# Performance work log

Hardware: AMD Instinct MI355X
Metric: run time of the kernel (lower is better)

The kernel has to match this reference:

```python
import jax, jax.numpy as jnp
import numpy as np

NUM_HEADS = 16
HEAD_SIZE = 64
EMB = NUM_HEADS * HEAD_SIZE
B, S = 2, 2048


def setup_inputs() -> dict:
    key = jax.random.key(0)
    ks = jax.random.split(key, 8)
    return {
        "values": jax.random.normal(ks[0], (B, S, EMB), dtype=jnp.float32),
        "keys": jax.random.normal(ks[1], (B, S, EMB), dtype=jnp.float32),
        "queries": jax.random.normal(ks[2], (B, S, EMB), dtype=jnp.float32),
        "mask": jnp.ones((B, 1, 1, S), dtype=jnp.int32),
        "Wq": jax.random.normal(ks[3], (HEAD_SIZE, HEAD_SIZE), dtype=jnp.float32) / np.sqrt(HEAD_SIZE),
        "Wk": jax.random.normal(ks[4], (HEAD_SIZE, HEAD_SIZE), dtype=jnp.float32) / np.sqrt(HEAD_SIZE),
        "Wv": jax.random.normal(ks[5], (HEAD_SIZE, HEAD_SIZE), dtype=jnp.float32) / np.sqrt(HEAD_SIZE),
        "Wout": jax.random.normal(ks[6], (EMB, EMB), dtype=jnp.float32) / np.sqrt(EMB),
        "bout": jax.random.normal(ks[7], (EMB,), dtype=jnp.float32) * 0.01,
    }


def reference(values, keys, queries, mask, Wq, Wk, Wv, Wout, bout):
    n, q_len, E = queries.shape
    H, D = NUM_HEADS, HEAD_SIZE
    # split heads: [n, len, H, D]
    v = values.reshape(n, -1, H, D)
    k = keys.reshape(n, -1, H, D)
    q = queries.reshape(n, q_len, H, D)
    # per-head shared linears (torch Linear: x @ W.T), no bias
    v = jnp.einsum("nkhd,cd->nkhc", v, Wv)
    k = jnp.einsum("nkhd,cd->nkhc", k, Wk)
    q = jnp.einsum("nqhd,cd->nqhc", q, Wq)
    # scores: [n, H, q, k]
    energy = jnp.einsum("nqhd,nkhd->nhqk", q, k)
    energy = jnp.where(mask == 0, jnp.float32(-1e28), energy)
    # NOTE: source scales by sqrt(embedding_size), not head_size
    attn = jax.nn.softmax(energy / jnp.sqrt(jnp.float32(E)), axis=3)
    out = jnp.einsum("nhqk,nkhd->nqhd", attn, v).reshape(n, q_len, E)
    return out @ Wout.T + bout
```

## Files before the change

kernel.cpp:

```cpp
#include <hip/hip_runtime.h>
#include <hip/hip_bf16.h>


#define NHB 16
#define HS  64
#define EMB 1024
#define BB  2
#define SS  2048
#define NT  (SS / 64)

typedef __bf16 bf16_t;
typedef bf16_t bf16x8 __attribute__((ext_vector_type(8)));
typedef bf16_t bf16x4 __attribute__((ext_vector_type(4)));
typedef float  f32x4  __attribute__((ext_vector_type(4)));

__device__ __forceinline__ f32x4 mfma16(bf16x8 a, bf16x8 b, f32x4 c) {
    return __builtin_amdgcn_mfma_f32_16x16x32_bf16(a, b, c, 0, 0, 0);
}

__global__ __launch_bounds__(256) void proj_kernel(
    const float* __restrict__ queries, const float* __restrict__ keys,
    const float* __restrict__ values,
    const float* __restrict__ Wq, const float* __restrict__ Wk,
    const float* __restrict__ Wv,
    bf16_t* __restrict__ Qb, bf16_t* __restrict__ Kb, bf16_t* __restrict__ Vt)
{
    __shared__ bf16_t Ws[3][64][72];
    __shared__ bf16_t Xs[64][72];

    const int tid  = threadIdx.x;
    const int wave = tid >> 6, lane = tid & 63;
    const int q4 = lane >> 4, l16 = lane & 15;
    const int s0 = blockIdx.x * 64;
    const int h  = blockIdx.y, n = blockIdx.z;

    for (int mW = 0; mW < 3; ++mW) {
        const float* wp = (mW == 0) ? Wq : (mW == 1) ? Wk : Wv;
        #pragma unroll
        for (int i = 0; i < 4; ++i) {
            int idx4 = i * 256 + tid;
            float4 v = ((const float4*)wp)[idx4];
            int r = idx4 >> 4, c = (idx4 & 15) * 4;
            Ws[mW][r][c+0] = (bf16_t)v.x; Ws[mW][r][c+1] = (bf16_t)v.y;
            Ws[mW][r][c+2] = (bf16_t)v.z; Ws[mW][r][c+3] = (bf16_t)v.w;
        }
    }

    const size_t headBase = (size_t)(n * NHB + h) * SS * HS;

    for (int p = 0; p < 3; ++p) {
        __syncthreads();
        const float* xp = (p == 0) ? queries : (p == 1) ? keys : values;
        #pragma unroll
        for (int i = 0; i < 4; ++i) {
            int idx4 = i * 256 + tid;
            int r = idx4 >> 4, c = (idx4 & 15) * 4;
            float4 v = *(const float4*)&xp[((size_t)(n * SS + s0 + r)) * EMB + h * HS + c];
            Xs[r][c+0] = (bf16_t)v.x; Xs[r][c+1] = (bf16_t)v.y;
            Xs[r][c+2] = (bf16_t)v.z; Xs[r][c+3] = (bf16_t)v.w;
        }
        __syncthreads();

        bf16x8 xf[2], wf[4][2];
        #pragma unroll
        for (int kk = 0; kk < 2; ++kk)
            xf[kk] = *(const bf16x8*)&Xs[wave * 16 + l16][kk * 32 + q4 * 8];
        #pragma unroll
        for (int ct = 0; ct < 4; ++ct)
            #pragma unroll
            for (int kk = 0; kk < 2; ++kk)
                wf[ct][kk] = *(const bf16x8*)&Ws[p][ct * 16 + l16][kk * 32 + q4 * 8];

        if (p < 2) {
            bf16_t* dst = (p == 0) ? Qb : Kb;
            const float sc = (p == 0) ? (0.03125f * 1.44269504f) : 1.0f;
            #pragma unroll
            for (int ct = 0; ct < 4; ++ct) {
                f32x4 acc = {};
                acc = mfma16(wf[ct][0], xf[0], acc);
                acc = mfma16(wf[ct][1], xf[1], acc);
                bf16x4 pk;
                #pragma unroll
                for (int i = 0; i < 4; ++i) pk[i] = (bf16_t)(acc[i] * sc);
                *(bf16x4*)&dst[headBase + (size_t)(s0 + wave * 16 + l16) * HS
                               + ct * 16 + q4 * 4] = pk;
            }
        } else {
            #pragma unroll
            for (int ct = 0; ct < 4; ++ct) {
                f32x4 acc = {};
                acc = mfma16(xf[0], wf[ct][0], acc);
                acc = mfma16(xf[1], wf[ct][1], acc);
                bf16x4 pk;
                #pragma unroll
                for (int i = 0; i < 4; ++i) pk[i] = (bf16_t)acc[i];
                *(bf16x4*)&Vt[headBase + (size_t)(ct * 16 + l16) * SS
                              + s0 + (wave >> 1) * 32 + q4 * 8 + (wave & 1) * 4] = pk;
            }
        }
    }
}

__global__ __launch_bounds__(256) void attn_kernel(
    const bf16_t* __restrict__ Qb, const bf16_t* __restrict__ Kb,
    const bf16_t* __restrict__ Vt, const int* __restrict__ mask,
    bf16_t* __restrict__ Og)
{
    __shared__ bf16_t Ks[2][64][72];
    __shared__ bf16_t Vs[2][64][72];
    __shared__ float  Ms[2][64];

    const int tid = threadIdx.x;
    const int w = tid >> 6, lane = tid & 63;
    const int q4 = lane >> 4, l16 = lane & 15;
    const int qt = blockIdx.x, h = blockIdx.y, n = blockIdx.z;
    const size_t headBase = (size_t)(n * NHB + h) * SS * HS;
    const int* mrow = mask + n * SS;

    const int sr0 = tid >> 3, sc0 = (tid & 7) * 8;
    const int sr1 = sr0 + 32;
    const bf16_t* kb0 = Kb + headBase + (size_t)sr0 * HS + sc0;
    const bf16_t* kb1 = Kb + headBase + (size_t)sr1 * HS + sc0;
    const bf16_t* vt0 = Vt + headBase + (size_t)sr0 * SS + sc0;
    const bf16_t* vt1 = Vt + headBase + (size_t)sr1 * SS + sc0;

    bf16x8 bq[2][2];
    #pragma unroll
    for (int st = 0; st < 2; ++st) {
        const bf16_t* qptr = Qb + headBase
            + (size_t)(qt * 128 + w * 32 + st * 16 + l16) * HS;
        bq[st][0] = *(const bf16x8*)&qptr[q4 * 8];
        bq[st][1] = *(const bf16x8*)&qptr[32 + q4 * 8];
    }

    f32x4 oaccT[2][4] = {};
    float lsum[2] = {0.f, 0.f};

    *(bf16x8*)&Ks[0][sr0][sc0] = *(const bf16x8*)kb0;
    *(bf16x8*)&Ks[0][sr1][sc0] = *(const bf16x8*)kb1;
    *(bf16x8*)&Vs[0][sr0][sc0] = *(const bf16x8*)vt0;
    *(bf16x8*)&Vs[0][sr1][sc0] = *(const bf16x8*)vt1;
    if (tid < 64) Ms[0][tid] = mrow[tid] ? 1.0f : 0.0f;
    __syncthreads();

    for (int kt = 0; kt < NT; ++kt) {
        const int cur = kt & 1;
        const bool has_next = (kt + 1) < NT;
        bf16x8 gk0, gk1, gv0, gv1; float gm = 0.f;
        if (has_next) {
            const int k0n = (kt + 1) * 64;
            gk0 = *(const bf16x8*)(kb0 + (size_t)k0n * HS);
            gk1 = *(const bf16x8*)(kb1 + (size_t)k0n * HS);
            gv0 = *(const bf16x8*)(vt0 + k0n);
            gv1 = *(const bf16x8*)(vt1 + k0n);
            if (tid < 64) gm = mrow[k0n + tid] ? 1.0f : 0.0f;
        }

        f32x4 sacc[2][4] = {};
        #pragma unroll
        for (int ct = 0; ct < 4; ++ct) {
            bf16x8 ak0 = *(const bf16x8*)&Ks[cur][ct * 16 + l16][q4 * 8];
            bf16x8 ak1 = *(const bf16x8*)&Ks[cur][ct * 16 + l16][32 + q4 * 8];
            #pragma unroll
            for (int st = 0; st < 2; ++st) {
                sacc[st][ct] = mfma16(ak0, bq[st][0], sacc[st][ct]);
                sacc[st][ct] = mfma16(ak1, bq[st][1], sacc[st][ct]);
            }
        }

        bf16x4 pv[2][4];
        #pragma unroll
        for (int ct = 0; ct < 4; ++ct) {
            float mf[4];
            *(float4*)mf = *(const float4*)&Ms[cur][ct * 16 + q4 * 4];
            #pragma unroll
            for (int st = 0; st < 2; ++st) {
                bf16x4 pk;
                #pragma unroll
                for (int j = 0; j < 4; ++j) {
                    float e = exp2f(sacc[st][ct][j]) * mf[j];
                    lsum[st] += e;
                    pk[j] = (bf16_t)e;
                }
                pv[st][ct] = pk;
            }
        }

        #pragma unroll
        for (int kb = 0; kb < 2; ++kb) {
            bf16x8 pa[2];
            #pragma unroll
            for (int st = 0; st < 2; ++st)
                pa[st] = __builtin_shufflevector(pv[st][2 * kb], pv[st][2 * kb + 1],
                                                 0, 1, 2, 3, 4, 5, 6, 7);
            #pragma unroll
            for (int dt = 0; dt < 4; ++dt) {
                bf16x8 av = *(const bf16x8*)&Vs[cur][dt * 16 + l16][kb * 32 + q4 * 8];
                #pragma unroll
                for (int st = 0; st < 2; ++st)
                    oaccT[st][dt] = mfma16(av, pa[st], oaccT[st][dt]);
            }
        }

        if (has_next) {
            const int nxt = 1 - cur;
            *(bf16x8*)&Ks[nxt][sr0][sc0] = gk0;
            *(bf16x8*)&Ks[nxt][sr1][sc0] = gk1;
            *(bf16x8*)&Vs[nxt][sr0][sc0] = gv0;
            *(bf16x8*)&Vs[nxt][sr1][sc0] = gv1;
            if (tid < 64) Ms[nxt][tid] = gm;
        }
        __syncthreads();
    }

    #pragma unroll
    for (int st = 0; st < 2; ++st) {
        float ls = lsum[st];
        ls += __shfl_xor(ls, 16, 64);
        ls += __shfl_xor(ls, 32, 64);
        const float inv = 1.f / ls;
        const int qrow = qt * 128 + w * 32 + st * 16 + l16;
        bf16_t* obase = Og + ((size_t)(n * SS + qrow)) * EMB + h * HS;
        #pragma unroll
        for (int dt = 0; dt < 4; ++dt) {
            bf16x4 ov;
            #pragma unroll
            for (int j = 0; j < 4; ++j) ov[j] = (bf16_t)(oaccT[st][dt][j] * inv);
            *(bf16x4*)&obase[dt * 16 + q4 * 4] = ov;
        }
    }
}

__global__ __launch_bounds__(256) void wconv_kernel(
    const float* __restrict__ W, bf16_t* __restrict__ Wb)
{
    int idx4 = blockIdx.x * 256 + threadIdx.x;
    float4 v = ((const float4*)W)[idx4];
    bf16x4 o;
    o[0] = (bf16_t)v.x; o[1] = (bf16_t)v.y; o[2] = (bf16_t)v.z; o[3] = (bf16_t)v.w;
    *(bf16x4*)&Wb[idx4 * 4] = o;
}

__global__ __launch_bounds__(512) void outproj_kernel(
    const bf16_t* __restrict__ Og, const bf16_t* __restrict__ Wb,
    const float* __restrict__ bout, float* __restrict__ out)
{
    __shared__ bf16_t As[2][128][72];
    __shared__ bf16_t Bs[2][128][72];
    const int tid = threadIdx.x;
    const int w = tid >> 6, lane = tid & 63;
    const int q4 = lane >> 4, l16 = lane & 15;
    const int wr = w >> 1, wc = w & 1;
    const int t0 = blockIdx.x * 128, c0 = blockIdx.y * 128;

    const int sr0 = tid >> 3, sc0 = (tid & 7) * 8;
    const int sr1 = sr0 + 64;
    const bf16_t* a0 = Og + (size_t)(t0 + sr0) * EMB + sc0;
    const bf16_t* a1 = Og + (size_t)(t0 + sr1) * EMB + sc0;
    const bf16_t* b0 = Wb + (size_t)(c0 + sr0) * EMB + sc0;
    const bf16_t* b1 = Wb + (size_t)(c0 + sr1) * EMB + sc0;

    f32x4 acc[2][4] = {};

    *(bf16x8*)&As[0][sr0][sc0] = *(const bf16x8*)a0;
    *(bf16x8*)&As[0][sr1][sc0] = *(const bf16x8*)a1;
    *(bf16x8*)&Bs[0][sr0][sc0] = *(const bf16x8*)b0;
    *(bf16x8*)&Bs[0][sr1][sc0] = *(const bf16x8*)b1;
    __syncthreads();

    const int NE = EMB / 64;
    for (int et = 0; et < NE; ++et) {
        const int cur = et & 1;
        const bool has_next = (et + 1) < NE;
        bf16x8 ga0, ga1, gb0, gb1;
        if (has_next) {
            const int e0 = (et + 1) * 64;
            ga0 = *(const bf16x8*)(a0 + e0); ga1 = *(const bf16x8*)(a1 + e0);
            gb0 = *(const bf16x8*)(b0 + e0); gb1 = *(const bf16x8*)(b1 + e0);
        }

        bf16x8 af[2][2], bfr[4][2];
        #pragma unroll
        for (int st = 0; st < 2; ++st)
            #pragma unroll
            for (int kk = 0; kk < 2; ++kk)
                af[st][kk] = *(const bf16x8*)&As[cur][wr * 32 + st * 16 + l16][kk * 32 + q4 * 8];
        #pragma unroll
        for (int ct = 0; ct < 4; ++ct)
            #pragma unroll
            for (int kk = 0; kk < 2; ++kk)
                bfr[ct][kk] = *(const bf16x8*)&Bs[cur][wc * 64 + ct * 16 + l16][kk * 32 + q4 * 8];
        #pragma unroll
        for (int st = 0; st < 2; ++st)
            #pragma unroll
            for (int ct = 0; ct < 4; ++ct) {
                acc[st][ct] = mfma16(af[st][0], bfr[ct][0], acc[st][ct]);
                acc[st][ct] = mfma16(af[st][1], bfr[ct][1], acc[st][ct]);
            }

        if (has_next) {
            const int nxt = 1 - cur;
            *(bf16x8*)&As[nxt][sr0][sc0] = ga0;
            *(bf16x8*)&As[nxt][sr1][sc0] = ga1;
            *(bf16x8*)&Bs[nxt][sr0][sc0] = gb0;
            *(bf16x8*)&Bs[nxt][sr1][sc0] = gb1;
        }
        __syncthreads();
    }

    #pragma unroll
    for (int ct = 0; ct < 4; ++ct) {
        const int c = c0 + wc * 64 + ct * 16 + l16;
        const float bias = bout[c];
        #pragma unroll
        for (int st = 0; st < 2; ++st)
            #pragma unroll
            for (int i = 0; i < 4; ++i)
                out[(size_t)(t0 + wr * 32 + st * 16 + q4 * 4 + i) * EMB + c]
                    = acc[st][ct][i] + bias;
    }
}

extern "C" void kernel_launch(void* const* d_in, const int* in_sizes, int n_in,
                              void* d_out, int out_size, void* d_ws, size_t ws_size,
                              hipStream_t stream)
{
    const float* values  = (const float*)d_in[0];
    const float* keys    = (const float*)d_in[1];
    const float* queries = (const float*)d_in[2];
    const int*   mask    = (const int*)d_in[3];
    const float* Wq      = (const float*)d_in[4];
    const float* Wk      = (const float*)d_in[5];
    const float* Wv      = (const float*)d_in[6];
    const float* Wout    = (const float*)d_in[7];
    const float* bout    = (const float*)d_in[8];
    float* out = (float*)d_out;

    const size_t M8 = 8ull * 1024 * 1024;
    bf16_t* Qb = (bf16_t*)d_ws;
    bf16_t* Kb = (bf16_t*)((char*)d_ws + 1 * M8);
    bf16_t* Vt = (bf16_t*)((char*)d_ws + 2 * M8);
    bf16_t* Og = (bf16_t*)((char*)d_ws + 3 * M8);
    bf16_t* Wb = Qb;

    proj_kernel<<<dim3(SS / 64, NHB, BB), 256, 0, stream>>>(
        queries, keys, values, Wq, Wk, Wv, Qb, Kb, Vt);
    attn_kernel<<<dim3(SS / 128, NHB, BB), 256, 0, stream>>>(
        Qb, Kb, Vt, mask, Og);
    wconv_kernel<<<dim3(1024), 256, 0, stream>>>(Wout, Wb);
    outproj_kernel<<<dim3((BB * SS) / 128, EMB / 128), 512, 0, stream>>>(
        Og, Wb, bout, out);
}
```

Before: 198.2 us.

## Split attention key tiles across two wave groups and shrink outproj column tile

The attention kernel now runs 512 threads per block. Two groups of four waves each handle half of every 64-key tile for the same query rows, and their partial outputs and row sums are combined through shared memory at the end. This doubles the waves available per block, since the grid has only 512 blocks, and cuts the per-wave MFMA chain in exchange for an extra reduction pass and barrier. The output projection halves its column tile to 64, which doubles its grid for better CU coverage but reloads the A operand more often.

Result: faster. 187.2 us (-5.5%).

```diff
diff --git a/kernel.cpp b/kernel.cpp
--- a/kernel.cpp
+++ b/kernel.cpp
@@ -101,34 +101,35 @@
     }
 }
 
-__global__ __launch_bounds__(256) void attn_kernel(
+__global__ __launch_bounds__(512) void attn_kernel(
     const bf16_t* __restrict__ Qb, const bf16_t* __restrict__ Kb,
     const bf16_t* __restrict__ Vt, const int* __restrict__ mask,
     bf16_t* __restrict__ Og)
 {
-    __shared__ bf16_t Ks[2][64][72];
-    __shared__ bf16_t Vs[2][64][72];
-    __shared__ float  Ms[2][64];
+    __shared__ __align__(16) unsigned char smem[37376];
+    auto Ks = (bf16_t(*)[64][72])(smem);
+    auto Vs = (bf16_t(*)[64][72])(smem + 18432);
+    auto Ms = (float(*)[64])(smem + 36864);
+    float* fbuf = (float*)smem;
+    float* lbuf = (float*)(smem + 32768);
 
     const int tid = threadIdx.x;
     const int w = tid >> 6, lane = tid & 63;
     const int q4 = lane >> 4, l16 = lane & 15;
+    const int wq = w & 3, wk = w >> 2;
     const int qt = blockIdx.x, h = blockIdx.y, n = blockIdx.z;
     const size_t headBase = (size_t)(n * NHB + h) * SS * HS;
     const int* mrow = mask + n * SS;
 
-    const int sr0 = tid >> 3, sc0 = (tid & 7) * 8;
-    const int sr1 = sr0 + 32;
-    const bf16_t* kb0 = Kb + headBase + (size_t)sr0 * HS + sc0;
-    const bf16_t* kb1 = Kb + headBase + (size_t)sr1 * HS + sc0;
-    const bf16_t* vt0 = Vt + headBase + (size_t)sr0 * SS + sc0;
-    const bf16_t* vt1 = Vt + headBase + (size_t)sr1 * SS + sc0;
+    const int sr = tid >> 3, sc = (tid & 7) * 8;
+    const bf16_t* kb_src = Kb + headBase + (size_t)sr * HS + sc;
+    const bf16_t* vt_src = Vt + headBase + (size_t)sr * SS + sc;
 
     bf16x8 bq[2][2];
     #pragma unroll
     for (int st = 0; st < 2; ++st) {
         const bf16_t* qptr = Qb + headBase
-            + (size_t)(qt * 128 + w * 32 + st * 16 + l16) * HS;
+            + (size_t)(qt * 128 + wq * 32 + st * 16 + l16) * HS;
         bq[st][0] = *(const bf16x8*)&qptr[q4 * 8];
         bq[st][1] = *(const bf16x8*)&qptr[32 + q4 * 8];
     }
@@ -136,41 +137,39 @@
     f32x4 oaccT[2][4] = {};
     float lsum[2] = {0.f, 0.f};
 
-    *(bf16x8*)&Ks[0][sr0][sc0] = *(const bf16x8*)kb0;
-    *(bf16x8*)&Ks[0][sr1][sc0] = *(const bf16x8*)kb1;
-    *(bf16x8*)&Vs[0][sr0][sc0] = *(const bf16x8*)vt0;
-    *(bf16x8*)&Vs[0][sr1][sc0] = *(const bf16x8*)vt1;
+    *(bf16x8*)&Ks[0][sr][sc] = *(const bf16x8*)kb_src;
+    *(bf16x8*)&Vs[0][sr][sc] = *(const bf16x8*)vt_src;
     if (tid < 64) Ms[0][tid] = mrow[tid] ? 1.0f : 0.0f;
     __syncthreads();
 
     for (int kt = 0; kt < NT; ++kt) {
         const int cur = kt & 1;
         const bool has_next = (kt + 1) < NT;
-        bf16x8 gk0, gk1, gv0, gv1; float gm = 0.f;
+        bf16x8 gk, gv; float gm = 0.f;
         if (has_next) {
             const int k0n = (kt + 1) * 64;
-            gk0 = *(const bf16x8*)(kb0 + (size_t)k0n * HS);
-            gk1 = *(const bf16x8*)(kb1 + (size_t)k0n * HS);
-            gv0 = *(const bf16x8*)(vt0 + k0n);
-            gv1 = *(const bf16x8*)(vt1 + k0n);
+            gk = *(const bf16x8*)(kb_src + (size_t)k0n * HS);
+            gv = *(const bf16x8*)(vt_src + k0n);
             if (tid < 64) gm = mrow[k0n + tid] ? 1.0f : 0.0f;
         }
 
-        f32x4 sacc[2][4] = {};
-        #pragma unroll
-        for (int ct = 0; ct < 4; ++ct) {
+        f32x4 sacc[2][2] = {};
+        #pragma unroll
+        for (int c2 = 0; c2 < 2; ++c2) {
+            const int ct = wk * 2 + c2;
             bf16x8 ak0 = *(const bf16x8*)&Ks[cur][ct * 16 + l16][q4 * 8];
             bf16x8 ak1 = *(const bf16x8*)&Ks[cur][ct * 16 + l16][32 + q4 * 8];
             #pragma unroll
             for (int st = 0; st < 2; ++st) {
-                sacc[st][ct] = mfma16(ak0, bq[st][0], sacc[st][ct]);
-                sacc[st][ct] = mfma16(ak1, bq[st][1], sacc[st][ct]);
-            }
-        }
-
-        bf16x4 pv[2][4];
-        #pragma unroll
-        for (int ct = 0; ct < 4; ++ct) {
+                sacc[st][c2] = mfma16(ak0, bq[st][0], sacc[st][c2]);
+                sacc[st][c2] = mfma16(ak1, bq[st][1], sacc[st][c2]);
+            }
+        }
+
+        bf16x4 pv[2][2];
+        #pragma unroll
+        for (int c2 = 0; c2 < 2; ++c2) {
+            const int ct = wk * 2 + c2;
             float mf[4];
             *(float4*)mf = *(const float4*)&Ms[cur][ct * 16 + q4 * 4];
             #pragma unroll
@@ -178,55 +177,80 @@
                 bf16x4 pk;
                 #pragma unroll
                 for (int j = 0; j < 4; ++j) {
-                    float e = exp2f(sacc[st][ct][j]) * mf[j];
+                    float e = exp2f(sacc[st][c2][j]) * mf[j];
                     lsum[st] += e;
                     pk[j] = (bf16_t)e;
                 }
-                pv[st][ct] = pk;
-            }
-        }
-
-        #pragma unroll
-        for (int kb = 0; kb < 2; ++kb) {
-            bf16x8 pa[2];
-            #pragma unroll
-            for (int st = 0; st < 2; ++st)
-                pa[st] = __builtin_shufflevector(pv[st][2 * kb], pv[st][2 * kb + 1],
-                                                 0, 1, 2, 3, 4, 5, 6, 7);
-            #pragma unroll
-            for (int dt = 0; dt < 4; ++dt) {
-                bf16x8 av = *(const bf16x8*)&Vs[cur][dt * 16 + l16][kb * 32 + q4 * 8];
-                #pragma unroll
-                for (int st = 0; st < 2; ++st)
-                    oaccT[st][dt] = mfma16(av, pa[st], oaccT[st][dt]);
-            }
+                pv[st][c2] = pk;
+            }
+        }
+
+        bf16x8 pa[2];
+        #pragma unroll
+        for (int st = 0; st < 2; ++st)
+            pa[st] = __builtin_shufflevector(pv[st][0], pv[st][1],
+                                             0, 1, 2, 3, 4, 5, 6, 7);
+        #pragma unroll
+        for (int dt = 0; dt < 4; ++dt) {
+            bf16x8 av = *(const bf16x8*)&Vs[cur][dt * 16 + l16][wk * 32 + q4 * 8];
+            oaccT[0][dt] = mfma16(av, pa[0], oaccT[0][dt]);
+            oaccT[1][dt] = mfma16(av, pa[1], oaccT[1][dt]);
         }
 
         if (has_next) {
             const int nxt = 1 - cur;
-            *(bf16x8*)&Ks[nxt][sr0][sc0] = gk0;
-            *(bf16x8*)&Ks[nxt][sr1][sc0] = gk1;
-            *(bf16x8*)&Vs[nxt][sr0][sc0] = gv0;
-            *(bf16x8*)&Vs[nxt][sr1][sc0] = gv1;
+            *(bf16x8*)&Ks[nxt][sr][sc] = gk;
+            *(bf16x8*)&Vs[nxt][sr][sc] = gv;
             if (tid < 64) Ms[nxt][tid] = gm;
         }
         __syncthreads();
     }
 
+    float ls[2];
     #pragma unroll
     for (int st = 0; st < 2; ++st) {
-        float ls = lsum[st];
-        ls += __shfl_xor(ls, 16, 64);
-        ls += __shfl_xor(ls, 32, 64);
-        const float inv = 1.f / ls;
-        const int qrow = qt * 128 + w * 32 + st * 16 + l16;
-        bf16_t* obase = Og + ((size_t)(n * SS + qrow)) * EMB + h * HS;
-        #pragma unroll
-        for (int dt = 0; dt < 4; ++dt) {
-            bf16x4 ov;
-            #pragma unroll
-            for (int j = 0; j < 4; ++j) ov[j] = (bf16_t)(oaccT[st][dt][j] * inv);
-            *(bf16x4*)&obase[dt * 16 + q4 * 4] = ov;
+        float v = lsum[st];
+        v += __shfl_xor(v, 16, 64);
+        v += __shfl_xor(v, 32, 64);
+        ls[st] = v;
+    }
+
+    if (w >= 4) {
+        const int lanecol = wq * 64 + lane;
+        #pragma unroll
+        for (int st = 0; st < 2; ++st) {
+            #pragma unroll
+            for (int dt = 0; dt < 4; ++dt)
+                #pragma unroll
+                for (int j = 0; j < 4; ++j)
+                    fbuf[(st * 16 + dt * 4 + j) * 256 + lanecol] = oaccT[st][dt][j];
+            lbuf[st * 256 + lanecol] = ls[st];
+        }
+    }
+    __syncthreads();
+    if (w < 4) {
+        const int lanecol = wq * 64 + lane;
+        #pragma unroll
+        for (int st = 0; st < 2; ++st) {
+            #pragma unroll
+            for (int dt = 0; dt < 4; ++dt)
+                #pragma unroll
+                for (int j = 0; j < 4; ++j)
+                    oaccT[st][dt][j] += fbuf[(st * 16 + dt * 4 + j) * 256 + lanecol];
+            ls[st] += lbuf[st * 256 + lanecol];
+        }
+        #pragma unroll
+        for (int st = 0; st < 2; ++st) {
+            const float inv = 1.f / ls[st];
+            const int qrow = qt * 128 + wq * 32 + st * 16 + l16;
+            bf16_t* obase = Og + ((size_t)(n * SS + qrow)) * EMB + h * HS;
+            #pragma unroll
+            for (int dt = 0; dt < 4; ++dt) {
+                bf16x4 ov;
+                #pragma unroll
+                for (int j = 0; j < 4; ++j) ov[j] = (bf16_t)(oaccT[st][dt][j] * inv);
+                *(bf16x4*)&obase[dt * 16 + q4 * 4] = ov;
+            }
         }
     }
 }
@@ -246,54 +270,52 @@
     const float* __restrict__ bout, float* __restrict__ out)
 {
     __shared__ bf16_t As[2][128][72];
-    __shared__ bf16_t Bs[2][128][72];
+    __shared__ bf16_t Bs[2][64][72];
     const int tid = threadIdx.x;
     const int w = tid >> 6, lane = tid & 63;
     const int q4 = lane >> 4, l16 = lane & 15;
     const int wr = w >> 1, wc = w & 1;
-    const int t0 = blockIdx.x * 128, c0 = blockIdx.y * 128;
+    const int t0 = blockIdx.x * 128, c0 = blockIdx.y * 64;
 
     const int sr0 = tid >> 3, sc0 = (tid & 7) * 8;
     const int sr1 = sr0 + 64;
     const bf16_t* a0 = Og + (size_t)(t0 + sr0) * EMB + sc0;
     const bf16_t* a1 = Og + (size_t)(t0 + sr1) * EMB + sc0;
     const bf16_t* b0 = Wb + (size_t)(c0 + sr0) * EMB + sc0;
-    const bf16_t* b1 = Wb + (size_t)(c0 + sr1) * EMB + sc0;
-
-    f32x4 acc[2][4] = {};
+
+    f32x4 acc[2][2] = {};
 
     *(bf16x8*)&As[0][sr0][sc0] = *(const bf16x8*)a0;
     *(bf16x8*)&As[0][sr1][sc0] = *(const bf16x8*)a1;
     *(bf16x8*)&Bs[0][sr0][sc0] = *(const bf16x8*)b0;
-    *(bf16x8*)&Bs[0][sr1][sc0] = *(const bf16x8*)b1;
     __syncthreads();
 
     const int NE = EMB / 64;
     for (int et = 0; et < NE; ++et) {
         const int cur = et & 1;
         const bool has_next = (et + 1) < NE;
-        bf16x8 ga0, ga1, gb0, gb1;
+        bf16x8 ga0, ga1, gb0;
         if (has_next) {
             const int e0 = (et + 1) * 64;
             ga0 = *(const bf16x8*)(a0 + e0); ga1 = *(const bf16x8*)(a1 + e0);
-            gb0 = *(const bf16x8*)(b0 + e0); gb1 = *(const bf16x8*)(b1 + e0);
-        }
-
-        bf16x8 af[2][2], bfr[4][2];
+            gb0 = *(const bf16x8*)(b0 + e0);
+        }
+
+        bf16x8 af[2][2], bfr[2][2];
         #pragma unroll
         for (int st = 0; st < 2; ++st)
             #pragma unroll
             for (int kk = 0; kk < 2; ++kk)
                 af[st][kk] = *(const bf16x8*)&As[cur][wr * 32 + st * 16 + l16][kk * 32 + q4 * 8];
         #pragma unroll
-        for (int ct = 0; ct < 4; ++ct)
+        for (int ct = 0; ct < 2; ++ct)
             #pragma unroll
             for (int kk = 0; kk < 2; ++kk)
-                bfr[ct][kk] = *(const bf16x8*)&Bs[cur][wc * 64 + ct * 16 + l16][kk * 32 + q4 * 8];
+                bfr[ct][kk] = *(const bf16x8*)&Bs[cur][wc * 32 + ct * 16 + l16][kk * 32 + q4 * 8];
         #pragma unroll
         for (int st = 0; st < 2; ++st)
             #pragma unroll
-            for (int ct = 0; ct < 4; ++ct) {
+            for (int ct = 0; ct < 2; ++ct) {
                 acc[st][ct] = mfma16(af[st][0], bfr[ct][0], acc[st][ct]);
                 acc[st][ct] = mfma16(af[st][1], bfr[ct][1], acc[st][ct]);
             }
@@ -303,14 +325,13 @@
             *(bf16x8*)&As[nxt][sr0][sc0] = ga0;
             *(bf16x8*)&As[nxt][sr1][sc0] = ga1;
             *(bf16x8*)&Bs[nxt][sr0][sc0] = gb0;
-            *(bf16x8*)&Bs[nxt][sr1][sc0] = gb1;
         }
         __syncthreads();
     }
 
     #pragma unroll
-    for (int ct = 0; ct < 4; ++ct) {
-        const int c = c0 + wc * 64 + ct * 16 + l16;
+    for (int ct = 0; ct < 2; ++ct) {
+        const int c = c0 + wc * 32 + ct * 16 + l16;
         const float bias = bout[c];
         #pragma unroll
         for (int st = 0; st < 2; ++st)
@@ -345,9 +366,9 @@
 
     proj_kernel<<<dim3(SS / 64, NHB, BB), 256, 0, stream>>>(
         queries, keys, values, Wq, Wk, Wv, Qb, Kb, Vt);
-    attn_kernel<<<dim3(SS / 128, NHB, BB), 256, 0, stream>>>(
+    attn_kernel<<<dim3(SS / 128, NHB, BB), 512, 0, stream>>>(
         Qb, Kb, Vt, mask, Og);
     wconv_kernel<<<dim3(1024), 256, 0, stream>>>(Wout, Wb);
-    outproj_kernel<<<dim3((BB * SS) / 128, EMB / 128), 512, 0, stream>>>(
+    outproj_kernel<<<dim3((BB * SS) / 128, EMB / 64), 512, 0, stream>>>(
         Og, Wb, bout, out);
 }
```
